# Kernel optimization log

Hardware: AMD Instinct MI355X
Metric: run time of the kernel (lower is better)

The kernel has to match this reference:

```python
import jax, jax.numpy as jnp
import numpy as np

INF = jnp.float32(1e9)


def _hungarian_min_perm(Cp, n):
    """Shortest-augmenting-path Hungarian (e-maxx variant) on padded cost Cp.
    Cp: (n+1, n+1) with Cp[i, j] = C[i-1, j-1] for i,j >= 1; row/col 0 virtual.
    Returns p: (n+1,) int32 where p[j] (j>=1) is the 1-based row assigned to col j.
    """
    cols = jnp.arange(n + 1)

    def outer(i, carry):
        u, v, p = carry
        p = p.at[0].set(i)
        init = (jnp.int32(0), u, v, p,
                jnp.full(n + 1, INF, Cp.dtype),
                jnp.zeros(n + 1, bool),
                jnp.zeros(n + 1, jnp.int32))

        def cond(s):
            j0, u, v, p, minv, used, way = s
            return p[j0] != 0

        def body(s):
            j0, u, v, p, minv, used, way = s
            used = used.at[j0].set(True)
            i0 = p[j0]
            cur = Cp[i0] - u[i0] - v                      # reduced costs, (n+1,)
            avail = (~used) & (cols >= 1)
            better = avail & (cur < minv)
            minv = jnp.where(better, cur, minv)
            way = jnp.where(better, j0, way)
            mv = jnp.where(avail, minv, INF)
            j1 = jnp.argmin(mv).astype(jnp.int32)
            delta = mv[j1]
            u = u.at[p].add(jnp.where(used, delta, 0.0))  # u[p[j]] += delta for used j
            v = v - jnp.where(used, delta, 0.0)
            minv = jnp.where(used, minv, minv - delta)
            return (j1, u, v, p, minv, used, way)

        j0, u, v, p, minv, used, way = jax.lax.while_loop(cond, body, init)

        # reconstruct augmenting path
        def cond2(s):
            return s[0] != 0

        def body2(s):
            j0, p = s
            j1 = way[j0]
            return (j1, p.at[j0].set(p[j1]))

        _, p = jax.lax.while_loop(cond2, body2, (j0, p))
        return (u, v, p)

    u0 = jnp.zeros(n + 1, Cp.dtype)
    v0 = jnp.zeros(n + 1, Cp.dtype)
    p0 = jnp.zeros(n + 1, jnp.int32)
    _, _, p = jax.lax.fori_loop(1, n + 1, outer, (u0, v0, p0))
    return p


def hungarian_maximize(a):
    """a: (n, n) benefit matrix -> (n, n) 0/1 optimal assignment matrix (maximize)."""
    n = a.shape[0]
    Cp = jnp.zeros((n + 1, n + 1), a.dtype).at[1:, 1:].set(-a)  # minimize -a
    p = _hungarian_min_perm(Cp, n)
    return jnp.zeros((n, n), jnp.float32).at[p[1:] - 1, jnp.arange(n)].set(1.0)


batched_lsa = jax.vmap(hungarian_maximize)


def setup_inputs() -> dict:
    key = jax.random.key(0)
    B, H, W = 1024, 128, 128
    x = jax.random.normal(key, (B, H, W), dtype=jnp.float32)
    bias = jnp.ones((H, W), dtype=jnp.float32)  # nn.Parameter(torch.ones(h, w))
    return {"x": x, "bias": bias}


def reference(x, bias):
    perm = batched_lsa(x)                               # (B, h, w) 0/1 assignments
    out = perm / jnp.sqrt(jnp.sum(perm * perm))         # global L2 norm (dim=None, keepdim)
    out = out * bias                                    # broadcast (h, w)
    return jax.nn.softmax(out, axis=2)                  # w >= h -> softmax over dim 2
```

## Files before the change

### kernel.cpp

```cpp
#include <hip/hip_runtime.h>
#include <hip/hip_fp16.h>

#define N 128
#define INF_ 1e9f
#define QNAN_U 0x7FC00000u
typedef unsigned long long ull;

__device__ __forceinline__ unsigned f2ord(float f) {
    unsigned b = __float_as_uint(f);
    return b ^ ((unsigned)((int)b >> 31) | 0x80000000u);
}
__device__ __forceinline__ float ord2f(unsigned k) {
    unsigned b = k ^ ((unsigned)((int)(~k) >> 31) | 0x80000000u);
    return __uint_as_float(b);
}
template <int CTRL>
__device__ __forceinline__ int dppmov(int v) {
    return __builtin_amdgcn_update_dpp(v, v, CTRL, 0xF, 0xF, false);
}
__device__ __forceinline__ int rl(int v, int lane) { return __builtin_amdgcn_readlane(v, lane); }
__device__ __forceinline__ unsigned rlu(unsigned v, int lane) {
    return (unsigned)__builtin_amdgcn_readlane((int)v, lane);
}
__device__ __forceinline__ float rlf(float v, int lane) {
    return __int_as_float(__builtin_amdgcn_readlane(__float_as_int(v), lane));
}
__device__ __forceinline__ unsigned uminu(unsigned a, unsigned b) { return a < b ? a : b; }

#define GMIN16(k) { \
    k = uminu(k, (unsigned)dppmov<0x121>((int)k)); \
    k = uminu(k, (unsigned)dppmov<0x122>((int)k)); \
    k = uminu(k, (unsigned)dppmov<0x124>((int)k)); \
    k = uminu(k, (unsigned)dppmov<0x128>((int)k)); \
}
#define GMINALL(k, gmin) { \
    unsigned _g0 = rlu(k, 0), _g1 = rlu(k, 16), _g2 = rlu(k, 32), _g3 = rlu(k, 48); \
    gmin = uminu(uminu(_g0, _g1), uminu(_g2, _g3)); \
}
#define RLPAIR_I(r0, r1, idx, dst) { \
    int _ln = ((idx) - 1) >> 1; \
    int _a = rl(r0, _ln), _b = rl(r1, _ln); \
    dst = (((idx) - 1) & 1) ? _b : _a; \
}

__global__ void __launch_bounds__(64) lsa_solve_kernel(
        const float* __restrict__ x, const float* __restrict__ bias,
        float* __restrict__ out, int B) {
    __shared__ unsigned Cs[N][64];
    __shared__ float u_lds[N + 1];
    __shared__ int   colOf[N + 1];
    __shared__ int   freeQ[N + 1];

    const int b = blockIdx.x;
    const int l = threadIdx.x;
    const int c0 = 2 * l + 1, c1 = 2 * l + 2;
    const ull mlt = (1ull << l) - 1;
    const float* xb = x + (size_t)b * (N * N);

    float m0 = INF_, m1 = INF_; int am0 = 1, am1 = 1;
    #pragma unroll 4
    for (int r = 0; r < N; ++r) {
        const float2 f = *(const float2*)&xb[r * N + 2 * l];
        __half2 h = __floats2half2_rn(-f.x, -f.y);
        Cs[r][l] = __builtin_bit_cast(unsigned, h);
        float f0 = __low2float(h), f1 = __high2float(h);
        if (f0 < m0) { m0 = f0; am0 = r + 1; }
        if (f1 < m1) { m1 = f1; am1 = r + 1; }
    }
    u_lds[l] = 0.f;   u_lds[l + 64] = 0.f;
    colOf[l + 1] = 0; colOf[l + 65] = 0;
    freeQ[l] = 0x7FFFFFFF; freeQ[l + 64] = 0x7FFFFFFF;
    if (l == 0) { u_lds[128] = 0.f; colOf[0] = 0; freeQ[128] = 0x7FFFFFFF; }
    __syncthreads();

    float v0r = m0, v1r = m1;
    atomicMin(&freeQ[am0], c0);
    atomicMin(&freeQ[am1], c1);
    __syncthreads();
    int prow0 = (freeQ[am0] == c0) ? am0 : 0;
    int prow1 = (freeQ[am1] == c1) ? am1 : 0;
    if (prow0) colOf[am0] = c0;
    if (prow1) colOf[am1] = c1;
    __syncthreads();

    {
        float pend0 = 0.f, pend1 = 0.f;
        #pragma unroll 2
        for (int r = 1; r <= N; ++r) {
            int j1 = __builtin_amdgcn_readfirstlane(colOf[r]);
            __half2 h = __builtin_bit_cast(__half2, Cs[r - 1][l]);
            float rc0 = __low2float(h)  - v0r;
            float rc1 = __high2float(h) - v1r;
            if (c0 == j1) rc0 = INF_;
            if (c1 == j1) rc1 = INF_;
            unsigned k = uminu(f2ord(rc0), f2ord(rc1));
            GMIN16(k)
            unsigned gmin; GMINALL(k, gmin)
            float m2 = ord2f(gmin);
            if (j1 != 0) {
                if (c0 == j1) pend0 = m2;
                if (c1 == j1) pend1 = m2;
            }
        }
        v0r -= pend0; v1r -= pend1;
    }

    int nf;
    {
        int fA = (colOf[l + 1] == 0);
        int fB = (colOf[l + 65] == 0);
        ull bA = __ballot(fA), bB = __ballot(fB);
        int nA = __popcll(bA);
        if (fA) freeQ[__popcll(bA & mlt)] = l + 1;
        if (fB) freeQ[nA + __popcll(bB & mlt)] = l + 65;
        nf = nA + __popcll(bB);
    }
    __syncthreads();

    {
        int budget = 4 * nf + 24;
        bool stop = false;
        #pragma unroll 1
        for (int kk = 0; kk < nf && !stop; ++kk) {
            int i = __builtin_amdgcn_readfirstlane(freeQ[kk]);
            #pragma unroll 1
            while (i != 0) {
                if (--budget < 0) { stop = true; break; }
                __half2 h = __builtin_bit_cast(__half2, Cs[i - 1][l]);
                float rc0 = __low2float(h)  - v0r;
                float rc1 = __high2float(h) - v1r;
                unsigned k0 = f2ord(rc0), k1 = f2ord(rc1);
                unsigned klm = uminu(k0, k1);
                int isHi = (k1 < k0) ? 1 : 0;
                unsigned kg = klm;
                GMIN16(kg)
                unsigned gmin; GMINALL(kg, gmin)
                ull bw = __ballot(klm == gmin);
                int wl = (int)__builtin_ctzll(bw);
                int hi1 = rl(isHi, wl);
                int j1 = 2 * wl + 1 + hi1;
                unsigned oth = (l == wl) ? (hi1 ? k0 : k1) : klm;
                unsigned kg2 = oth;
                GMIN16(kg2)
                unsigned m2o; GMINALL(kg2, m2o)
                if (gmin < m2o) {
                    float d = ord2f(m2o) - ord2f(gmin);
                    if (c0 == j1) v0r -= d;
                    if (c1 == j1) v1r -= d;
                } else {
                    int pj1; RLPAIR_I(prow0, prow1, j1, pj1)
                    if (pj1 != 0) {
                        ull bw2 = __ballot(oth == m2o);
                        int wl2 = (int)__builtin_ctzll(bw2);
                        int hi2 = (wl2 == wl) ? (hi1 ^ 1) : rl(isHi, wl2);
                        j1 = 2 * wl2 + 1 + hi2;
                    }
                }
                int disp; RLPAIR_I(prow0, prow1, j1, disp)
                if (c0 == j1) prow0 = i;
                if (c1 == j1) prow1 = i;
                if (l == 0) {
                    colOf[i] = j1;
                    if (disp != 0) colOf[disp] = 0;
                }
                i = disp;
            }
        }
        __syncthreads();
    }

    {
        int fA = (colOf[l + 1] == 0);
        int fB = (colOf[l + 65] == 0);
        ull bA = __ballot(fA), bB = __ballot(fB);
        int nA = __popcll(bA);
        if (fA) freeQ[__popcll(bA & mlt)] = l + 1;
        if (fB) freeQ[nA + __popcll(bB & mlt)] = l + 65;
        nf = nA + __popcll(bB);
    }
    __syncthreads();
    int qv0 = freeQ[l], qv1 = freeQ[l + 64];

    #pragma unroll 1
    for (int fi = 0; fi < nf; ++fi) {
        int sl = fi & 63;
        const int i = (fi < 64) ? rl(qv0, sl) : rl(qv1, sl);
        __half2 h = __builtin_bit_cast(__half2, Cs[i - 1][l]);
        float rc0 = __low2float(h)  - v0r;
        float rc1 = __high2float(h) - v1r;
        unsigned k0 = f2ord(rc0), k1 = f2ord(rc1);
        unsigned kl = uminu(k0, k1);
        int isHi = (k1 < k0) ? 1 : 0;
        unsigned kg = kl;
        GMIN16(kg)
        unsigned gmin; GMINALL(kg, gmin)
        ull bw = __ballot(kl == gmin);
        int wl = (int)__builtin_ctzll(bw);
        int hi = rl(isHi, wl);
        int jm = 2 * wl + 1 + hi;
        if (l == 0) u_lds[i] = ord2f(gmin);
        int pm; RLPAIR_I(prow0, prow1, jm, pm)
        if (pm == 0) {
            if (c0 == jm) prow0 = i;
            if (c1 == jm) prow1 = i;
            if (l == 0) colOf[i] = jm;
        }
    }
    __syncthreads();

    if (prow0) {
        __half2 h = __builtin_bit_cast(__half2, Cs[prow0 - 1][l]);
        u_lds[prow0] = __low2float(h) - v0r;
    }
    if (prow1) {
        __half2 h = __builtin_bit_cast(__half2, Cs[prow1 - 1][l]);
        u_lds[prow1] = __high2float(h) - v1r;
    }
    __syncthreads();

    {
        int fA = (colOf[l + 1] == 0);
        int fB = (colOf[l + 65] == 0);
        ull bA = __ballot(fA), bB = __ballot(fB);
        int nA = __popcll(bA);
        if (fA) freeQ[__popcll(bA & mlt)] = l + 1;
        if (fB) freeQ[nA + __popcll(bB & mlt)] = l + 65;
        nf = nA + __popcll(bB);
    }
    __syncthreads();
    qv0 = freeQ[l]; qv1 = freeQ[l + 64];
    float uprow0 = u_lds[prow0], uprow1 = u_lds[prow1];

    unsigned nrootw = 0; float nu = 0.f;
    if (nf > 0) {
        int i0f = rl(qv0, 0);
        nrootw = Cs[i0f - 1][l];
        nu = u_lds[i0f];
    }

    #pragma unroll 1
    for (int fi = 0; fi < nf; ++fi) {
        int sl = fi & 63;
        const int i = (fi < 64) ? rl(qv0, sl) : rl(qv1, sl);

        float dist0 = INF_, dist1 = INF_;
        int   way0 = 0, way1 = 0;
        float cumAt0 = 0.f, cumAt1 = 0.f;
        float cum = 0.f;
        float base = -nu;
        int   jcur = 0, i0 = i;
        unsigned roww = nrootw;

        #pragma unroll 1
        for (int it = 0; it <= N; ++it) {
            float t0 = base - v0r, t1 = base - v1r;
            if (c0 == jcur) { cumAt0 = cum; dist0 = __int_as_float(QNAN_U); }
            if (c1 == jcur) { cumAt1 = cum; dist1 = __int_as_float(QNAN_U); }

            __half2 h = __builtin_bit_cast(__half2, roww);
            float cand0 = __low2float(h)  + t0;
            float cand1 = __high2float(h) + t1;
            if (cand0 < dist0) { dist0 = cand0; way0 = jcur; }
            if (cand1 < dist1) { dist1 = cand1; way1 = jcur; }

            unsigned k0 = f2ord(dist0), k1 = f2ord(dist1);
            unsigned kl = uminu(k0, k1);
            int isHi = (k1 < k0) ? 1 : 0;
            int   pay  = isHi ? ((1 << 8) | prow1) : prow0;
            float upay = isHi ? uprow1 : uprow0;
            unsigned kg = kl;
            GMIN16(kg)
            unsigned gmin; GMINALL(kg, gmin)
            ull bw = __ballot(kl == gmin);
            int wl = (int)__builtin_ctzll(bw);
            int payw = rl(pay, wl);
            float uw = rlf(upay, wl);
            cum  = ord2f(gmin);
            jcur = 2 * wl + 1 + ((payw >> 8) & 1);
            i0   = payw & 0xFF;
            base = cum - uw;
            if (i0 == 0) break;
            roww = Cs[i0 - 1][l];
        }

        if (fi + 1 < nf) {
            int slp = (fi + 1) & 63;
            int inx = (fi + 1 < 64) ? rl(qv0, slp) : rl(qv1, slp);
            nrootw = Cs[inx - 1][l];
            nu = u_lds[inx];
        }

        bool used0 = (__float_as_uint(dist0) == QNAN_U);
        bool used1 = (__float_as_uint(dist1) == QNAN_U);
        if (used0) { float dv = cum - cumAt0; v0r -= dv; u_lds[prow0] += dv; }
        if (used1) { float dv = cum - cumAt1; v1r -= dv; u_lds[prow1] += dv; }
        if (l == 0) u_lds[i] += cum;
        __syncthreads();

        int j = jcur;
        #pragma unroll 1
        while (j != 0) {
            int idx = j - 1, slw = idx >> 1, hib = idx & 1;
            int w0 = rl(way0, slw), w1 = rl(way1, slw);
            int jn = hib ? w1 : w0;
            int pn;
            if (jn == 0) pn = i;
            else {
                int pidx = jn - 1, slp2 = pidx >> 1, phb = pidx & 1;
                int p0 = rl(prow0, slp2), p1 = rl(prow1, slp2);
                pn = phb ? p1 : p0;
            }
            if (c0 == j) prow0 = pn;
            if (c1 == j) prow1 = pn;
            j = jn;
        }
        uprow0 = u_lds[prow0];
        uprow1 = u_lds[prow1];
    }

    colOf[prow0] = c0;
    colOf[prow1] = c1;
    __syncthreads();

    const float inv_norm = rsqrtf((float)B * (float)N);
    float* ob = out + (size_t)b * (N * N);
    #pragma unroll 2
    for (int r = 0; r < N; ++r) {
        int jA = __builtin_amdgcn_readfirstlane(colOf[r + 1]);
        float s = bias[r * N + (jA - 1)] * inv_norm;
        float e = __expf(s);
        float inv_d = 1.0f / (127.0f + e);
        float av = e * inv_d;
        float2 w;
        w.x = (c0 == jA) ? av : inv_d;
        w.y = (c1 == jA) ? av : inv_d;
        *(float2*)&ob[r * N + 2 * l] = w;
    }
}

extern "C" void kernel_launch(void* const* d_in, const int* in_sizes, int n_in,
                              void* d_out, int out_size, void* d_ws, size_t ws_size,
                              hipStream_t stream) {
    const float* x    = (const float*)d_in[0];
    const float* bias = (const float*)d_in[1];
    float* out = (float*)d_out;
    int B = in_sizes[0] / (N * N);
    hipLaunchKernelGGL(lsa_solve_kernel, dim3(B), dim3(64), 0, stream, x, bias, out, B);
}
```

Before: 320.0 us.

## Speculatively compute old-dist argmin and prefetch its row in Dijkstra loop

Splits each augmenting-path step's wavefront argmin into two independent reductions: one over the existing dist values, which does not depend on the newly loaded row, and one over the new candidates. The LDS row for the old-min winner is loaded speculatively so it overlaps the candidate reduction. The row-minimum scan is moved into a separate pass over LDS, the greedy budget is reduced, and the cross-iteration root prefetch is removed. The cost is a second full cross-lane reduction and an extra LDS load per step.

Result: slower. 436.7 us (+36.5%).

```diff
diff --git a/kernel.cpp b/kernel.cpp
--- a/kernel.cpp
+++ b/kernel.cpp
@@ -57,15 +57,11 @@
     const ull mlt = (1ull << l) - 1;
     const float* xb = x + (size_t)b * (N * N);
 
-    float m0 = INF_, m1 = INF_; int am0 = 1, am1 = 1;
     #pragma unroll 4
     for (int r = 0; r < N; ++r) {
         const float2 f = *(const float2*)&xb[r * N + 2 * l];
         __half2 h = __floats2half2_rn(-f.x, -f.y);
         Cs[r][l] = __builtin_bit_cast(unsigned, h);
-        float f0 = __low2float(h), f1 = __high2float(h);
-        if (f0 < m0) { m0 = f0; am0 = r + 1; }
-        if (f1 < m1) { m1 = f1; am1 = r + 1; }
     }
     u_lds[l] = 0.f;   u_lds[l + 64] = 0.f;
     colOf[l + 1] = 0; colOf[l + 65] = 0;
@@ -73,6 +69,14 @@
     if (l == 0) { u_lds[128] = 0.f; colOf[0] = 0; freeQ[128] = 0x7FFFFFFF; }
     __syncthreads();
 
+    float m0 = INF_, m1 = INF_; int am0 = 1, am1 = 1;
+    #pragma unroll 4
+    for (int r = 0; r < N; ++r) {
+        __half2 h = __builtin_bit_cast(__half2, Cs[r][l]);
+        float f0 = __low2float(h), f1 = __high2float(h);
+        if (f0 < m0) { m0 = f0; am0 = r + 1; }
+        if (f1 < m1) { m1 = f1; am1 = r + 1; }
+    }
     float v0r = m0, v1r = m1;
     atomicMin(&freeQ[am0], c0);
     atomicMin(&freeQ[am1], c1);
@@ -118,7 +122,7 @@
     __syncthreads();
 
     {
-        int budget = 4 * nf + 24;
+        int budget = 3 * nf + 16;
         bool stop = false;
         #pragma unroll 1
         for (int kk = 0; kk < nf && !stop; ++kk) {
@@ -231,13 +235,6 @@
     qv0 = freeQ[l]; qv1 = freeQ[l + 64];
     float uprow0 = u_lds[prow0], uprow1 = u_lds[prow1];
 
-    unsigned nrootw = 0; float nu = 0.f;
-    if (nf > 0) {
-        int i0f = rl(qv0, 0);
-        nrootw = Cs[i0f - 1][l];
-        nu = u_lds[i0f];
-    }
-
     #pragma unroll 1
     for (int fi = 0; fi < nf; ++fi) {
         int sl = fi & 63;
@@ -247,47 +244,66 @@
         int   way0 = 0, way1 = 0;
         float cumAt0 = 0.f, cumAt1 = 0.f;
         float cum = 0.f;
-        float base = -nu;
+        float base = -u_lds[i];
         int   jcur = 0, i0 = i;
-        unsigned roww = nrootw;
+        unsigned roww = Cs[i - 1][l];
 
         #pragma unroll 1
         for (int it = 0; it <= N; ++it) {
-            float t0 = base - v0r, t1 = base - v1r;
             if (c0 == jcur) { cumAt0 = cum; dist0 = __int_as_float(QNAN_U); }
             if (c1 == jcur) { cumAt1 = cum; dist1 = __int_as_float(QNAN_U); }
 
+            unsigned k0o = f2ord(dist0), k1o = f2ord(dist1);
+            unsigned klo = uminu(k0o, k1o);
+            int isHiO = (k1o < k0o) ? 1 : 0;
+            int   payO  = isHiO ? ((1 << 8) | prow1) : prow0;
+            float upayO = isHiO ? uprow1 : uprow0;
+            unsigned kgo = klo;
+            GMIN16(kgo)
+            unsigned gOld; GMINALL(kgo, gOld)
+            ull bwo = __ballot(klo == gOld);
+            int wlo_ = (int)__builtin_ctzll(bwo);
+            int payow = rl(payO, wlo_);
+            float uOld = rlf(upayO, wlo_);
+            int jOld = 2 * wlo_ + 1 + ((payow >> 8) & 1);
+            int iOld = payow & 0xFF;
+            unsigned wspec = Cs[(iOld > 0 ? iOld : 1) - 1][l];
+
+            float t0 = base - v0r, t1 = base - v1r;
             __half2 h = __builtin_bit_cast(__half2, roww);
             float cand0 = __low2float(h)  + t0;
             float cand1 = __high2float(h) + t1;
-            if (cand0 < dist0) { dist0 = cand0; way0 = jcur; }
-            if (cand1 < dist1) { dist1 = cand1; way1 = jcur; }
-
-            unsigned k0 = f2ord(dist0), k1 = f2ord(dist1);
-            unsigned kl = uminu(k0, k1);
-            int isHi = (k1 < k0) ? 1 : 0;
-            int   pay  = isHi ? ((1 << 8) | prow1) : prow0;
-            float upay = isHi ? uprow1 : uprow0;
-            unsigned kg = kl;
-            GMIN16(kg)
-            unsigned gmin; GMINALL(kg, gmin)
-            ull bw = __ballot(kl == gmin);
-            int wl = (int)__builtin_ctzll(bw);
-            int payw = rl(pay, wl);
-            float uw = rlf(upay, wl);
-            cum  = ord2f(gmin);
-            jcur = 2 * wl + 1 + ((payw >> 8) & 1);
-            i0   = payw & 0xFF;
-            base = cum - uw;
+            if (__float_as_uint(dist0) == QNAN_U) cand0 = __int_as_float(QNAN_U);
+            if (__float_as_uint(dist1) == QNAN_U) cand1 = __int_as_float(QNAN_U);
+
+            unsigned k0c = f2ord(cand0), k1c = f2ord(cand1);
+            unsigned klc = uminu(k0c, k1c);
+            int isHiC = (k1c < k0c) ? 1 : 0;
+            int   payC  = isHiC ? ((1 << 8) | prow1) : prow0;
+            float upayC = isHiC ? uprow1 : uprow0;
+            unsigned kgc = klc;
+            GMIN16(kgc)
+            unsigned gCand; GMINALL(kgc, gCand)
+            ull bwc = __ballot(klc == gCand);
+            int wlc_ = (int)__builtin_ctzll(bwc);
+            int paycw = rl(payC, wlc_);
+            float uCand = rlf(upayC, wlc_);
+            int jCand = 2 * wlc_ + 1 + ((paycw >> 8) & 1);
+            int iCand = paycw & 0xFF;
+
+            bool oldwin = (gOld < gCand) || (gOld == gCand && jOld < jCand);
+            int jprev = jcur;
+            cum  = ord2f(oldwin ? gOld : gCand);
+            jcur = oldwin ? jOld : jCand;
+            i0   = oldwin ? iOld : iCand;
+            base = cum - (oldwin ? uOld : uCand);
+
+            if (cand0 < dist0) { dist0 = cand0; way0 = jprev; }
+            if (cand1 < dist1) { dist1 = cand1; way1 = jprev; }
+
             if (i0 == 0) break;
-            roww = Cs[i0 - 1][l];
-        }
-
-        if (fi + 1 < nf) {
-            int slp = (fi + 1) & 63;
-            int inx = (fi + 1 < 64) ? rl(qv0, slp) : rl(qv1, slp);
-            nrootw = Cs[inx - 1][l];
-            nu = u_lds[inx];
+            if (oldwin) roww = wspec;
+            else        roww = Cs[i0 - 1][l];
         }
 
         bool used0 = (__float_as_uint(dist0) == QNAN_U);
@@ -306,8 +322,8 @@
             int pn;
             if (jn == 0) pn = i;
             else {
-                int pidx = jn - 1, slp2 = pidx >> 1, phb = pidx & 1;
-                int p0 = rl(prow0, slp2), p1 = rl(prow1, slp2);
+                int pidx = jn - 1, slp = pidx >> 1, phb = pidx & 1;
+                int p0 = rl(prow0, slp), p1 = rl(prow1, slp);
                 pn = phb ? p1 : p0;
             }
             if (c0 == j) prow0 = pn;
```
